# Optimization experiments

Measured on AMD Instinct MI355X. Metric: run time of the kernel, lower is better.

## Reference

```python
import jax, jax.numpy as jnp
import numpy as np

B, S, D = 8, 1024, 512          # batch, seq_len, d_model
H, HD = 8, 64                   # num_heads, head_dim (D = H*HD)
L = 128                         # latent_dim
LH = L // H                     # latent_head_dim = 16
M_ALPHA = -1e9                  # additive mask coefficient


def setup_inputs() -> dict:
    key = jax.random.key(0)
    ks = jax.random.split(key, 9)
    s = 0.02
    return {
        "x": jax.random.normal(ks[0], (B, S, D), jnp.float32),
        "mask": jax.random.uniform(ks[1], (B, S, 1), jnp.float32),  # (B,S,1) single-column mask
        "Wq": jax.random.normal(ks[2], (D, D), jnp.float32) * s,
        "bq": jnp.zeros((D,), jnp.float32),
        "Wckv": jax.random.normal(ks[3], (D, L), jnp.float32) * s,   # latent KV compression
        "Wuk": jax.random.normal(ks[4], (L, D), jnp.float32) * s,    # key up-proj (absorbed into q)
        "Wuv": jax.random.normal(ks[5], (L, D), jnp.float32) * s,    # value up-proj
        "Wo": jax.random.normal(ks[6], (D, D), jnp.float32) * s,
        "bo": jnp.zeros((D,), jnp.float32),
    }


def reference(x, mask, Wq, bq, Wckv, Wuk, Wuv, Wo, bo):
    b, s, d = x.shape
    # Q path: full query then project into latent space via Wuk^T (weight absorption)
    q_full = x @ Wq + bq                              # (B,S,D)
    q_lat = q_full @ Wuk.T                            # (B,S,L)
    q = q_lat.reshape(b, s, H, LH).transpose(0, 2, 1, 3)      # (B,H,S,LH)
    # K/V path: compressed latent KV
    k_lat_full = x @ Wckv                             # (B,S,L)
    k = k_lat_full.reshape(b, s, H, LH).transpose(0, 2, 1, 3)  # (B,H,S,LH)
    v_full = k_lat_full @ Wuv                         # (B,S,D)
    v = v_full.reshape(b, s, H, HD).transpose(0, 2, 1, 3)      # (B,H,S,HD)
    # scaled dot-product in latent space (dk = latent_head_dim)
    logits = jnp.einsum('bhqd,bhkd->bhqk', q, k) / jnp.sqrt(jnp.float32(LH))
    qk_values = logits
    # 'QK' mask: tile single-column (B,S,1)->(B,S,S), symmetrize, clamp at 1
    m = jnp.broadcast_to(mask, (b, s, s))             # tile along keys
    m = m + m.transpose(0, 2, 1)                      # symmetric (square case)
    m = jnp.minimum(1.0, m)
    logits = logits + m[:, None, :, :] * M_ALPHA      # (B,H,S,S)
    attn_weights = jax.nn.softmax(logits, axis=-1)
    attn = jnp.einsum('bhqk,bhkd->bhqd', attn_weights, v)      # (B,H,S,HD)
    attn = attn.transpose(0, 2, 1, 3).reshape(b, s, d)         # merge heads
    out = attn @ Wo + bo                              # (B,S,D)
    return out, attn_weights, qk_values
```

## Files before the change

### kernel.cpp

```cpp
#include <hip/hip_runtime.h>
#include <hip/hip_bf16.h>

typedef __hip_bfloat16 bf16;
typedef __attribute__((ext_vector_type(8))) short short8;
typedef __attribute__((ext_vector_type(4))) float f32x4;

#define B_ 8
#define S_ 1024
#define D_ 512
#define H_ 8
#define HD_ 64
#define L_ 128
#define LH_ 16

__device__ __forceinline__ float bfu2f(unsigned short u) {
  unsigned int x = ((unsigned int)u) << 16;
  float f;
  __builtin_memcpy(&f, &x, 4);
  return f;
}
__device__ __forceinline__ unsigned short bfbits(float f) {
  bf16 h = __float2bfloat16(f);
  unsigned short u;
  __builtin_memcpy(&u, &h, 2);
  return u;
}
__device__ __forceinline__ f32x4 mfma_bf16(short8 a, short8 b, f32x4 c) {
  return __builtin_amdgcn_mfma_f32_16x16x32_bf16(a, b, c, 0, 0, 0);
}


template<bool BT, bool BIAS, bool ABF16, bool CBF16>
__global__ __launch_bounds__(256) void gemm(const void* __restrict__ Ap, int lda,
                                            const void* __restrict__ Bp, int ldb,
                                            void* __restrict__ Cp, int ldc,
                                            const float* __restrict__ bias, int K) {
  __shared__ float As[16][65];
  __shared__ float Bs[16][65];
  const int tid = threadIdx.x;
  const int m0 = blockIdx.y * 64, n0 = blockIdx.x * 64;
  const int ty = tid >> 4, tx = tid & 15;
  float acc[4][4] = {};
  for (int kt = 0; kt < K; kt += 16) {
    {
      const int m = tid >> 2, kq = (tid & 3) * 4;
      if (ABF16) {
        const bf16* A = (const bf16*)Ap;
        ushort4 u = *reinterpret_cast<const ushort4*>(
            reinterpret_cast<const unsigned short*>(A) + (size_t)(m0 + m) * lda + kt + kq);
        As[kq + 0][m] = bfu2f(u.x);
        As[kq + 1][m] = bfu2f(u.y);
        As[kq + 2][m] = bfu2f(u.z);
        As[kq + 3][m] = bfu2f(u.w);
      } else {
        const float* A = (const float*)Ap;
        float4 v = *reinterpret_cast<const float4*>(A + (size_t)(m0 + m) * lda + kt + kq);
        As[kq + 0][m] = v.x;
        As[kq + 1][m] = v.y;
        As[kq + 2][m] = v.z;
        As[kq + 3][m] = v.w;
      }
    }
    if (BT) {
      const int n = tid >> 2, kq = (tid & 3) * 4;
      const float* Bf = (const float*)Bp;
      float4 v = *reinterpret_cast<const float4*>(Bf + (size_t)(n0 + n) * ldb + kt + kq);
      Bs[kq + 0][n] = v.x;
      Bs[kq + 1][n] = v.y;
      Bs[kq + 2][n] = v.z;
      Bs[kq + 3][n] = v.w;
    } else {
      const int k = tid >> 4, nq = (tid & 15) * 4;
      const float* Bf = (const float*)Bp;
      float4 v = *reinterpret_cast<const float4*>(Bf + (size_t)(kt + k) * ldb + n0 + nq);
      Bs[k][nq + 0] = v.x;
      Bs[k][nq + 1] = v.y;
      Bs[k][nq + 2] = v.z;
      Bs[k][nq + 3] = v.w;
    }
    __syncthreads();
#pragma unroll
    for (int k = 0; k < 16; ++k) {
      float a0 = As[k][ty * 4 + 0], a1 = As[k][ty * 4 + 1];
      float a2 = As[k][ty * 4 + 2], a3 = As[k][ty * 4 + 3];
      float b0 = Bs[k][tx * 4 + 0], b1 = Bs[k][tx * 4 + 1];
      float b2 = Bs[k][tx * 4 + 2], b3 = Bs[k][tx * 4 + 3];
      acc[0][0] += a0 * b0; acc[0][1] += a0 * b1; acc[0][2] += a0 * b2; acc[0][3] += a0 * b3;
      acc[1][0] += a1 * b0; acc[1][1] += a1 * b1; acc[1][2] += a1 * b2; acc[1][3] += a1 * b3;
      acc[2][0] += a2 * b0; acc[2][1] += a2 * b1; acc[2][2] += a2 * b2; acc[2][3] += a2 * b3;
      acc[3][0] += a3 * b0; acc[3][1] += a3 * b1; acc[3][2] += a3 * b2; acc[3][3] += a3 * b3;
    }
    __syncthreads();
  }
#pragma unroll
  for (int i = 0; i < 4; ++i)
#pragma unroll
    for (int j = 0; j < 4; ++j) {
      const size_t row = m0 + ty * 4 + i;
      const int col = n0 + tx * 4 + j;
      float v = acc[i][j];
      if (BIAS) v += bias[col];
      if (CBF16)
        reinterpret_cast<bf16*>(Cp)[row * ldc + col] = __float2bfloat16(v);
      else
        reinterpret_cast<float*>(Cp)[row * ldc + col] = v;
    }
}

__global__ __launch_bounds__(256) void k_tr_f32(const float* __restrict__ in,
                                                float* __restrict__ out, int R, int C) {
  __shared__ float t[32][33];
  int tx = threadIdx.x & 31, ty = threadIdx.x >> 5;
  int r0 = blockIdx.y * 32, c0 = blockIdx.x * 32;
#pragma unroll
  for (int i = 0; i < 32; i += 8)
    t[ty + i][tx] = in[(size_t)(r0 + ty + i) * C + c0 + tx];
  __syncthreads();
#pragma unroll
  for (int i = 0; i < 32; i += 8)
    out[(size_t)(c0 + ty + i) * R + r0 + tx] = t[tx][ty + i];
}

__global__ __launch_bounds__(256) void k_tr_f32_bf16(const float* __restrict__ in,
                                                     bf16* __restrict__ out,
                                                     int R, int C) {
  __shared__ float t[32][33];
  int tx = threadIdx.x & 31, ty = threadIdx.x >> 5;
  int r0 = blockIdx.y * 32, c0 = blockIdx.x * 32;
#pragma unroll
  for (int i = 0; i < 32; i += 8)
    t[ty + i][tx] = in[(size_t)(r0 + ty + i) * C + c0 + tx];
  __syncthreads();
#pragma unroll
  for (int i = 0; i < 32; i += 8)
    out[(size_t)(c0 + ty + i) * R + r0 + tx] = __float2bfloat16(t[tx][ty + i]);
}

__global__ __launch_bounds__(256) void k_copy_wckv(const float* __restrict__ Wckv,
                                                   float* __restrict__ wcat) {
  int idx = blockIdx.x * 256 + threadIdx.x;
  int k = idx >> 7, n = idx & 127;
  wcat[k * 256 + 128 + n] = Wckv[k * 128 + n];
}

__global__ __launch_bounds__(64) void k_biascomb(const float* __restrict__ bq,
                                                 const float* __restrict__ Wuk,
                                                 float* __restrict__ bias_c) {
  int j = blockIdx.x, lane = threadIdx.x;
  if (j >= L_) { if (lane == 0) bias_c[j] = 0.f; return; }
  float s = 0.f;
  for (int d = lane; d < D_; d += 64) s += bq[d] * Wuk[j * D_ + d];
#pragma unroll
  for (int off = 32; off > 0; off >>= 1) s += __shfl_down(s, off);
  if (lane == 0) bias_c[j] = s;
}

__global__ __launch_bounds__(256) void k_qk3(const float* __restrict__ xw,
                                             const float* __restrict__ maskg,
                                             float* __restrict__ qk_out,
                                             float* __restrict__ aw_out) {
  __shared__ __align__(16) float Kl[512 * 20];
  __shared__ float mkl[S_];
  __shared__ float qls[8 * 16];
  const int bh = blockIdx.y, b = bh >> 3, h = bh & 7;
  const int q0 = blockIdx.x * 8;
  const int tid = threadIdx.x, w = tid >> 6, lane = tid & 63;

  for (int i = tid; i < S_; i += 256) mkl[i] = maskg[b * S_ + i];
  if (tid < 32) {
    const int row = tid >> 2, qq = (tid & 3) * 4;
    float4 v = *reinterpret_cast<const float4*>(
        xw + (size_t)(b * S_ + q0 + row) * 256 + h * LH_ + qq);
    qls[row * 16 + qq + 0] = v.x; qls[row * 16 + qq + 1] = v.y;
    qls[row * 16 + qq + 2] = v.z; qls[row * 16 + qq + 3] = v.w;
  }
  __syncthreads();

  const int r0 = w * 2;
  float qr[2][16], mq[2];
#pragma unroll
  for (int r = 0; r < 2; ++r) {
#pragma unroll
    for (int t = 0; t < 16; ++t) qr[r][t] = qls[(r0 + r) * 16 + t];
    mq[r] = mkl[q0 + r0 + r];
  }
  const size_t obase = (size_t)bh * S_ * S_;
  float l[2][16];

#pragma unroll
  for (int half = 0; half < 2; ++half) {
    if (half) __syncthreads();
#pragma unroll
    for (int i = 0; i < 8; ++i) {
      const int idx = tid + i * 256;
      const int key = idx >> 2, qq = (idx & 3) * 4;
      float4 v = *reinterpret_cast<const float4*>(
          xw + (size_t)(b * S_ + half * 512 + key) * 256 + 128 + h * LH_ + qq);
      *reinterpret_cast<float4*>(&Kl[key * 20 + qq]) = v;
    }
    __syncthreads();
#pragma unroll
    for (int c = 0; c < 8; ++c) {
      const int lkey = c * 64 + lane;
      const int key = half * 512 + lkey;
      float kv[16];
#pragma unroll
      for (int t = 0; t < 16; t += 4) {
        float4 v = *reinterpret_cast<const float4*>(&Kl[lkey * 20 + t]);
        kv[t] = v.x; kv[t + 1] = v.y; kv[t + 2] = v.z; kv[t + 3] = v.w;
      }
      const float mk = mkl[key];
#pragma unroll
      for (int r = 0; r < 2; ++r) {
        float d = 0.f;
#pragma unroll
        for (int t = 0; t < 16; ++t) d += qr[r][t] * kv[t];
        d *= 0.25f;
        qk_out[obase + (size_t)(q0 + r0 + r) * S_ + key] = d;
        const float m = fminf(1.f, __fadd_rn(mq[r], mk));
        l[r][half * 8 + c] = __fadd_rn(d, __fmul_rn(m, -1e9f));
      }
    }
  }

#pragma unroll
  for (int r = 0; r < 2; ++r) {
    float M = l[r][0];
#pragma unroll
    for (int idx = 1; idx < 16; ++idx) M = fmaxf(M, l[r][idx]);
#pragma unroll
    for (int st = 1; st < 64; st <<= 1) M = fmaxf(M, __shfl_xor(M, st));
    float s = 0.f;
#pragma unroll
    for (int idx = 0; idx < 16; ++idx) {
      const float e = __expf(l[r][idx] - M);
      l[r][idx] = e;
      s += e;
    }
#pragma unroll
    for (int st = 1; st < 64; st <<= 1) s += __shfl_xor(s, st);
    const float inv = 1.f / s;
    const size_t orow = obase + (size_t)(q0 + r0 + r) * S_;
#pragma unroll
    for (int idx = 0; idx < 16; ++idx)
      aw_out[orow + (idx >> 3) * 512 + (idx & 7) * 64 + lane] = l[r][idx] * inv;
  }
}

__global__ __launch_bounds__(256) void k_pv_mfma(const float* __restrict__ aw,
                                                 const bf16* __restrict__ vt,
                                                 bf16* __restrict__ attn) {
  __shared__ __align__(16) short Pl[128 * 40];
  __shared__ __align__(16) short Vl[64 * 40];
  const int bh = blockIdx.y, b = bh >> 3, h = bh & 7;
  const int q0 = blockIdx.x * 128;
  const int tid = threadIdx.x, w = tid >> 6, lane = tid & 63;
  const int l15 = lane & 15, l4 = lane >> 4;
  const float* A = aw + (size_t)bh * S_ * S_;
  const unsigned short* vtp =
      reinterpret_cast<const unsigned short*>(vt) + (size_t)h * 64 * 8192 + b * S_;
  f32x4 acc[2][4] = {};
  for (int kt = 0; kt < 32; ++kt) {
    __syncthreads();
    {
      const int r = tid >> 1, half = (tid & 1) * 16;
      const float* src = A + (size_t)(q0 + r) * S_ + kt * 32 + half;
      short* dst = &Pl[r * 40 + half];
#pragma unroll
      for (int i = 0; i < 4; ++i) {
        float4 v = *reinterpret_cast<const float4*>(src + i * 4);
        ushort4 o = { bfbits(v.x), bfbits(v.y), bfbits(v.z), bfbits(v.w) };
        *reinterpret_cast<ushort4*>(dst + i * 4) = o;
      }
    }
    if (tid < 64) {
      const unsigned short* src = vtp + (size_t)tid * 8192 + kt * 32;
      *reinterpret_cast<uint4*>(&Vl[tid * 40 + 0])  = *reinterpret_cast<const uint4*>(src + 0);
      *reinterpret_cast<uint4*>(&Vl[tid * 40 + 8])  = *reinterpret_cast<const uint4*>(src + 8);
      *reinterpret_cast<uint4*>(&Vl[tid * 40 + 16]) = *reinterpret_cast<const uint4*>(src + 16);
      *reinterpret_cast<uint4*>(&Vl[tid * 40 + 24]) = *reinterpret_cast<const uint4*>(src + 24);
    }
    __syncthreads();
    short8 av[2], bv[4];
#pragma unroll
    for (int mf = 0; mf < 2; ++mf)
      av[mf] = *reinterpret_cast<const short8*>(&Pl[(w * 32 + mf * 16 + l15) * 40 + l4 * 8]);
#pragma unroll
    for (int nf = 0; nf < 4; ++nf)
      bv[nf] = *reinterpret_cast<const short8*>(&Vl[(nf * 16 + l15) * 40 + l4 * 8]);
#pragma unroll
    for (int mf = 0; mf < 2; ++mf)
#pragma unroll
      for (int nf = 0; nf < 4; ++nf)
        acc[mf][nf] = mfma_bf16(av[mf], bv[nf], acc[mf][nf]);
  }
#pragma unroll
  for (int mf = 0; mf < 2; ++mf)
#pragma unroll
    for (int nf = 0; nf < 4; ++nf)
#pragma unroll
      for (int j = 0; j < 4; ++j)
        attn[(size_t)(b * S_ + q0 + w * 32 + mf * 16 + l4 * 4 + j) * 512 +
             h * 64 + nf * 16 + l15] = __float2bfloat16(acc[mf][nf][j]);
}

__global__ __launch_bounds__(256) void gemm_mfma_out(const bf16* __restrict__ Ab,
                                                     const bf16* __restrict__ Bt,
                                                     float* __restrict__ C,
                                                     const float* __restrict__ bias) {
  __shared__ __align__(16) short sA[128 * 40];
  __shared__ __align__(16) short sB[128 * 40];
  const int tid = threadIdx.x, lane = tid & 63;
  const int l15 = lane & 15, l4 = lane >> 4;
  const int wm = ((tid >> 6) >> 1) * 64, wn = ((tid >> 6) & 1) * 64;
  const size_t bn0 = (size_t)blockIdx.x * 128, bm0 = (size_t)blockIdx.y * 128;
  const unsigned short* A = reinterpret_cast<const unsigned short*>(Ab);
  const unsigned short* Bu = reinterpret_cast<const unsigned short*>(Bt);
  f32x4 acc[4][4] = {};
  for (int kt = 0; kt < 512; kt += 32) {
    __syncthreads();
#pragma unroll
    for (int i = 0; i < 2; ++i) {
      const int c = tid + i * 256;
      const int row = c >> 2, k8 = (c & 3) * 8;
      *reinterpret_cast<uint4*>(&sA[row * 40 + k8]) =
          *reinterpret_cast<const uint4*>(A + (bm0 + row) * 512 + kt + k8);
      *reinterpret_cast<uint4*>(&sB[row * 40 + k8]) =
          *reinterpret_cast<const uint4*>(Bu + (bn0 + row) * 512 + kt + k8);
    }
    __syncthreads();
    short8 av[4], bv[4];
#pragma unroll
    for (int mf = 0; mf < 4; ++mf)
      av[mf] = *reinterpret_cast<const short8*>(&sA[(wm + mf * 16 + l15) * 40 + l4 * 8]);
#pragma unroll
    for (int nf = 0; nf < 4; ++nf)
      bv[nf] = *reinterpret_cast<const short8*>(&sB[(wn + nf * 16 + l15) * 40 + l4 * 8]);
#pragma unroll
    for (int mf = 0; mf < 4; ++mf)
#pragma unroll
      for (int nf = 0; nf < 4; ++nf)
        acc[mf][nf] = mfma_bf16(av[mf], bv[nf], acc[mf][nf]);
  }
#pragma unroll
  for (int mf = 0; mf < 4; ++mf)
#pragma unroll
    for (int nf = 0; nf < 4; ++nf)
#pragma unroll
      for (int j = 0; j < 4; ++j) {
        const size_t row = bm0 + wm + mf * 16 + l4 * 4 + j;
        const int col = bn0 + wn + nf * 16 + l15;
        C[row * 512 + col] = acc[mf][nf][j] + bias[col];
      }
}

extern "C" void kernel_launch(void* const* d_in, const int* in_sizes, int n_in,
                              void* d_out, int out_size, void* d_ws, size_t ws_size,
                              hipStream_t stream) {
  const float* x    = (const float*)d_in[0];
  const float* mask = (const float*)d_in[1];
  const float* Wq   = (const float*)d_in[2];
  const float* bq   = (const float*)d_in[3];
  const float* Wckv = (const float*)d_in[4];
  const float* Wuk  = (const float*)d_in[5];
  const float* Wuv  = (const float*)d_in[6];
  const float* Wo   = (const float*)d_in[7];
  const float* bo   = (const float*)d_in[8];

  float* out    = (float*)d_out;
  float* aw_out = out + (size_t)B_ * S_ * D_;
  float* qk_out = aw_out + (size_t)B_ * H_ * S_ * S_;

  uint8_t* p = (uint8_t*)d_ws;
  auto alloc = [&](size_t bytes) {
    void* r = p;
    p += (bytes + 255) & ~(size_t)255;
    return r;
  };
  float* wcat    = (float*)alloc((size_t)512 * 256 * 4);
  float* bias_c  = (float*)alloc(256 * 4);
  float* wuvT_f  = (float*)alloc((size_t)512 * 128 * 4);
  bf16*  woT     = (bf16*)alloc((size_t)512 * 512 * 2);
  float* xw      = (float*)alloc((size_t)8192 * 256 * 4);
  bf16*  vt      = (bf16*)alloc((size_t)512 * 8192 * 2);
  bf16*  attn_bf = (bf16*)xw;

  gemm<true, false, false, false><<<dim3(2, 8), 256, 0, stream>>>(
      Wq, 512, Wuk, 512, wcat, 256, nullptr, 512);
  k_copy_wckv<<<256, 256, 0, stream>>>(Wckv, wcat);
  k_biascomb<<<256, 64, 0, stream>>>(bq, Wuk, bias_c);
  k_tr_f32<<<dim3(16, 4), 256, 0, stream>>>(Wuv, wuvT_f, 128, 512);
  k_tr_f32_bf16<<<dim3(16, 16), 256, 0, stream>>>(Wo, woT, 512, 512);
  gemm<false, true, false, false><<<dim3(4, 128), 256, 0, stream>>>(
      x, 512, wcat, 256, xw, 256, bias_c, 512);
  gemm<true, false, false, true><<<dim3(128, 8), 256, 0, stream>>>(
      wuvT_f, 128, xw + 128, 256, vt, 8192, nullptr, 128);
  k_qk3<<<dim3(128, 64), 256, 0, stream>>>(xw, mask, qk_out, aw_out);
  k_pv_mfma<<<dim3(8, 64), 256, 0, stream>>>(aw_out, vt, attn_bf);
  gemm_mfma_out<<<dim3(4, 64), 256, 0, stream>>>(attn_bf, woT, out, bo);
  (void)in_sizes; (void)n_in; (void)out_size; (void)ws_size;
}
```

Measured before the change: 374.3 us.

## Move latent projection and value up-projection GEMMs to bf16 MFMA

Replaces the two fp32 SIMT tiled GEMMs (x·[Wq·Wukᵀ | Wckv] and the transposed value up-projection) with a new templated bf16 MFMA GEMM using 128x128 tiles. Adds kernels to convert x and the projected latents to bf16, and transposes the weights into bf16. The aim is to move the projection work onto matrix cores. In exchange it adds extra conversion passes and workspace buffers, and it lowers input precision for q/k latents, which feed the exported qk_values and softmax weights.

```diff
diff --git a/kernel.cpp b/kernel.cpp
--- a/kernel.cpp
+++ b/kernel.cpp
@@ -107,18 +107,13 @@
     }
 }
 
-__global__ __launch_bounds__(256) void k_tr_f32(const float* __restrict__ in,
-                                                float* __restrict__ out, int R, int C) {
-  __shared__ float t[32][33];
-  int tx = threadIdx.x & 31, ty = threadIdx.x >> 5;
-  int r0 = blockIdx.y * 32, c0 = blockIdx.x * 32;
-#pragma unroll
-  for (int i = 0; i < 32; i += 8)
-    t[ty + i][tx] = in[(size_t)(r0 + ty + i) * C + c0 + tx];
-  __syncthreads();
-#pragma unroll
-  for (int i = 0; i < 32; i += 8)
-    out[(size_t)(c0 + ty + i) * R + r0 + tx] = t[tx][ty + i];
+__global__ __launch_bounds__(256) void k_conv(const float* __restrict__ in,
+                                              bf16* __restrict__ out, int n) {
+  int i = (blockIdx.x * 256 + threadIdx.x) * 4;
+  if (i >= n) return;
+  float4 v = *reinterpret_cast<const float4*>(in + i);
+  ushort4 o = { bfbits(v.x), bfbits(v.y), bfbits(v.z), bfbits(v.w) };
+  *reinterpret_cast<ushort4*>(out + i) = o;
 }
 
 __global__ __launch_bounds__(256) void k_tr_f32_bf16(const float* __restrict__ in,
@@ -153,6 +148,62 @@
 #pragma unroll
   for (int off = 32; off > 0; off >>= 1) s += __shfl_down(s, off);
   if (lane == 0) bias_c[j] = s;
+}
+
+template<int LDA, int LDB, int LDC, int KK, bool CBF16, bool BIAS>
+__global__ __launch_bounds__(256) void gemm_mfma_t(const bf16* __restrict__ Ab,
+                                                   const bf16* __restrict__ Bt,
+                                                   void* __restrict__ Cp,
+                                                   const float* __restrict__ bias) {
+  __shared__ __align__(16) short sA[128 * 40];
+  __shared__ __align__(16) short sB[128 * 40];
+  const int tid = threadIdx.x, lane = tid & 63;
+  const int l15 = lane & 15, l4 = lane >> 4;
+  const int wm = ((tid >> 6) >> 1) * 64, wn = ((tid >> 6) & 1) * 64;
+  const size_t bn0 = (size_t)blockIdx.x * 128, bm0 = (size_t)blockIdx.y * 128;
+  const unsigned short* A = reinterpret_cast<const unsigned short*>(Ab);
+  const unsigned short* Bu = reinterpret_cast<const unsigned short*>(Bt);
+  f32x4 acc[4][4] = {};
+  for (int kt = 0; kt < KK; kt += 32) {
+    __syncthreads();
+#pragma unroll
+    for (int i = 0; i < 2; ++i) {
+      const int c = tid + i * 256;
+      const int row = c >> 2, k8 = (c & 3) * 8;
+      *reinterpret_cast<uint4*>(&sA[row * 40 + k8]) =
+          *reinterpret_cast<const uint4*>(A + (bm0 + row) * LDA + kt + k8);
+      *reinterpret_cast<uint4*>(&sB[row * 40 + k8]) =
+          *reinterpret_cast<const uint4*>(Bu + (bn0 + row) * LDB + kt + k8);
+    }
+    __syncthreads();
+    short8 av[4], bv[4];
+#pragma unroll
+    for (int mf = 0; mf < 4; ++mf)
+      av[mf] = *reinterpret_cast<const short8*>(&sA[(wm + mf * 16 + l15) * 40 + l4 * 8]);
+#pragma unroll
+    for (int nf = 0; nf < 4; ++nf)
+      bv[nf] = *reinterpret_cast<const short8*>(&sB[(wn + nf * 16 + l15) * 40 + l4 * 8]);
+#pragma unroll
+    for (int mf = 0; mf < 4; ++mf)
+#pragma unroll
+      for (int nf = 0; nf < 4; ++nf)
+        acc[mf][nf] = mfma_bf16(av[mf], bv[nf], acc[mf][nf]);
+  }
+#pragma unroll
+  for (int mf = 0; mf < 4; ++mf)
+#pragma unroll
+    for (int nf = 0; nf < 4; ++nf)
+#pragma unroll
+      for (int j = 0; j < 4; ++j) {
+        const size_t row = bm0 + wm + mf * 16 + l4 * 4 + j;
+        const int col = bn0 + wn + nf * 16 + l15;
+        float v = acc[mf][nf][j];
+        if (BIAS) v += bias[col];
+        if (CBF16)
+          reinterpret_cast<bf16*>(Cp)[row * LDC + col] = __float2bfloat16(v);
+        else
+          reinterpret_cast<float*>(Cp)[row * LDC + col] = v;
+      }
 }
 
 __global__ __launch_bounds__(256) void k_qk3(const float* __restrict__ xw,
@@ -379,9 +430,12 @@
   };
   float* wcat    = (float*)alloc((size_t)512 * 256 * 4);
   float* bias_c  = (float*)alloc(256 * 4);
-  float* wuvT_f  = (float*)alloc((size_t)512 * 128 * 4);
+  bf16*  wcatT   = (bf16*)alloc((size_t)256 * 512 * 2);
+  bf16*  wuvT_bf = (bf16*)alloc((size_t)512 * 128 * 2);
   bf16*  woT     = (bf16*)alloc((size_t)512 * 512 * 2);
+  bf16*  x_bf    = (bf16*)alloc((size_t)8192 * 512 * 2);
   float* xw      = (float*)alloc((size_t)8192 * 256 * 4);
+  bf16*  xw_bf   = (bf16*)alloc((size_t)8192 * 256 * 2);
   bf16*  vt      = (bf16*)alloc((size_t)512 * 8192 * 2);
   bf16*  attn_bf = (bf16*)xw;
 
@@ -389,12 +443,15 @@
       Wq, 512, Wuk, 512, wcat, 256, nullptr, 512);
   k_copy_wckv<<<256, 256, 0, stream>>>(Wckv, wcat);
   k_biascomb<<<256, 64, 0, stream>>>(bq, Wuk, bias_c);
-  k_tr_f32<<<dim3(16, 4), 256, 0, stream>>>(Wuv, wuvT_f, 128, 512);
+  k_tr_f32_bf16<<<dim3(8, 16), 256, 0, stream>>>(wcat, wcatT, 512, 256);
+  k_tr_f32_bf16<<<dim3(16, 4), 256, 0, stream>>>(Wuv, wuvT_bf, 128, 512);
   k_tr_f32_bf16<<<dim3(16, 16), 256, 0, stream>>>(Wo, woT, 512, 512);
-  gemm<false, true, false, false><<<dim3(4, 128), 256, 0, stream>>>(
-      x, 512, wcat, 256, xw, 256, bias_c, 512);
-  gemm<true, false, false, true><<<dim3(128, 8), 256, 0, stream>>>(
-      wuvT_f, 128, xw + 128, 256, vt, 8192, nullptr, 128);
+  k_conv<<<4096, 256, 0, stream>>>(x, x_bf, 8192 * 512);
+  gemm_mfma_t<512, 512, 256, 512, false, true><<<dim3(2, 64), 256, 0, stream>>>(
+      x_bf, wcatT, xw, bias_c);
+  k_conv<<<2048, 256, 0, stream>>>(xw, xw_bf, 8192 * 256);
+  gemm_mfma_t<128, 256, 8192, 128, true, false><<<dim3(64, 4), 256, 0, stream>>>(
+      wuvT_bf, xw_bf + 128, vt, nullptr);
   k_qk3<<<dim3(128, 64), 256, 0, stream>>>(xw, mask, qk_out, aw_out);
   k_pv_mfma<<<dim3(8, 64), 256, 0, stream>>>(aw_out, vt, attn_bf);
   gemm_mfma_out<<<dim3(4, 64), 256, 0, stream>>>(attn_bf, woT, out, bo);
```

New measurement: 325.4 us. 13.1% less time.
